# Kernel optimization log

Measured on AMD Instinct MI355X. Metric: run time of the kernel, lower is better.

Reference implementation:

```python
import jax, jax.numpy as jnp
import numpy as np

# e2m1 FP4 value table: sign bit in nibble MSB, values {0,0.5,1,1.5,2,3,4,6}
_E2M1 = jnp.array([0.0, 0.5, 1.0, 1.5, 2.0, 3.0, 4.0, 6.0,
                   -0.0, -0.5, -1.0, -1.5, -2.0, -3.0, -4.0, -6.0], dtype=jnp.float32)


def _dequant_fp4(packed, scales, group_size):
    """packed: [E, out, in//8] uint32; scales: [E, in//group_size, out] -> [E, out, in] f32."""
    shifts = jnp.arange(8, dtype=jnp.uint32) * 4  # nibble shift amounts 0,4,...,28
    nib = (packed[..., None] >> shifts) & jnp.uint32(0xF)  # [E, out, in//8, 8]
    E, O, P, _ = nib.shape
    nib = nib.reshape(E, O, P * 8).astype(jnp.int32)
    w = _E2M1[nib]  # [E, out, in] f32
    gids = jnp.arange(P * 8) // group_size  # group id per input column
    sc = jnp.transpose(scales, (0, 2, 1))[:, :, gids]  # [E, out, in]
    return w * sc


def setup_inputs() -> dict:
    E, H, I, T, K, G = 8, 2048, 1408, 2048, 2, 128
    key = jax.random.key(0)
    ks = jax.random.split(key, 9)
    x = jax.random.normal(ks[0], (T, H), dtype=jnp.float32)
    gate_packed = jax.random.bits(ks[1], (E, I, H // 8), dtype=jnp.uint32)
    up_packed = jax.random.bits(ks[2], (E, I, H // 8), dtype=jnp.uint32)
    down_packed = jax.random.bits(ks[3], (E, H, I // 8), dtype=jnp.uint32)
    gate_scales = jax.random.uniform(ks[4], (E, H // G, I), jnp.float32, 0.5, 1.5)
    up_scales = jax.random.uniform(ks[5], (E, H // G, I), jnp.float32, 0.5, 1.5)
    down_scales = jax.random.uniform(ks[6], (E, I // G, H), jnp.float32, 0.5, 1.5)
    topk_idx = jax.random.randint(ks[7], (T, K), 0, E, dtype=jnp.int32)
    w = jax.random.uniform(ks[8], (T, K), jnp.float32)
    topk_w = w / jnp.sum(w, axis=-1, keepdims=True)
    return {"x": x,
            "gate_packed": gate_packed, "gate_scales": gate_scales,
            "up_packed": up_packed, "up_scales": up_scales,
            "down_packed": down_packed, "down_scales": down_scales,
            "topk_idx": topk_idx, "topk_w": topk_w, "group_size": G}


def reference(x, gate_packed, gate_scales, up_packed, up_scales,
              down_packed, down_scales, topk_idx, topk_w, group_size):
    # Fused dequant (nibble unpack + e2m1 table + per-group scale) for all experts
    gate_w = _dequant_fp4(gate_packed, gate_scales, group_size)  # [E, I, H]
    up_w = _dequant_fp4(up_packed, up_scales, group_size)        # [E, I, H]
    down_w = _dequant_fp4(down_packed, down_scales, group_size)  # [E, H, I]
    # Grouped SwiGLU expert MLP (dense over E=8 experts, gather routed outputs)
    g = jnp.einsum('th,eih->eti', x, gate_w)
    u = jnp.einsum('th,eih->eti', x, up_w)
    h = jax.nn.silu(g) * u                                        # [E, T, I]
    y = jnp.einsum('eti,ehi->eth', h, down_w)                     # [E, T, H]
    T = x.shape[0]
    sel = y[topk_idx, jnp.arange(T)[:, None], :]                  # [T, K, H]
    return jnp.sum(sel * topk_w[..., None], axis=1)               # [T, H]
```

## Files before the change

### kernel.cpp

```cpp
#include <hip/hip_runtime.h>
#include <hip/hip_bf16.h>
#include <stdint.h>

#define E_ 8
#define H_ 2048
#define I_ 1408
#define T_ 2048
#define K_ 2
#define G_ 128

typedef __bf16 bf16;
typedef bf16 bf16x8 __attribute__((ext_vector_type(8)));
typedef float f32x4 __attribute__((ext_vector_type(4)));

__device__ __forceinline__ uint32_t prm(uint32_t hi, uint32_t lo, uint32_t sel) {
    return __builtin_amdgcn_perm(hi, lo, sel);
}

struct DequantTab { uint32_t thi0, thi1, tlo0, tlo1; };

__device__ __forceinline__ DequantTab build_tab(float s) {
    union { bf16 h[8]; uint32_t u[4]; } tb;
    tb.h[0] = (bf16)(0.0f);
    tb.h[1] = (bf16)(0.5f * s);
    tb.h[2] = (bf16)(1.0f * s);
    tb.h[3] = (bf16)(1.5f * s);
    tb.h[4] = (bf16)(2.0f * s);
    tb.h[5] = (bf16)(3.0f * s);
    tb.h[6] = (bf16)(4.0f * s);
    tb.h[7] = (bf16)(6.0f * s);
    DequantTab t;
    t.thi0 = prm(tb.u[1], tb.u[0], 0x07050301u);
    t.tlo0 = prm(tb.u[1], tb.u[0], 0x06040200u);
    t.thi1 = prm(tb.u[3], tb.u[2], 0x07050301u);
    t.tlo1 = prm(tb.u[3], tb.u[2], 0x06040200u);
    return t;
}

__device__ __forceinline__ uint4 dequant8t(uint32_t p, const DequantTab& t) {
    const uint32_t pr = p >> 4;
    const uint32_t pe = p  & 0x07070707u;
    const uint32_t po = pr & 0x07070707u;
    const uint32_t He = prm(t.thi1, t.thi0, pe) | ((p  & 0x08080808u) << 4);
    const uint32_t Le = prm(t.tlo1, t.tlo0, pe);
    const uint32_t Ho = prm(t.thi1, t.thi0, po) | ((pr & 0x08080808u) << 4);
    const uint32_t Lo = prm(t.tlo1, t.tlo0, po);
    const uint32_t E01 = prm(He, Le, 0x05010400u);
    const uint32_t E23 = prm(He, Le, 0x07030602u);
    const uint32_t O01 = prm(Ho, Lo, 0x05010400u);
    const uint32_t O23 = prm(Ho, Lo, 0x07030602u);
    return make_uint4(prm(O01, E01, 0x05040100u),
                      prm(O01, E01, 0x07060302u),
                      prm(O23, E23, 0x05040100u),
                      prm(O23, E23, 0x07060302u));
}

__device__ __forceinline__ void gld16(void* lds, const void* g) {
    __builtin_amdgcn_global_load_lds(
        (__attribute__((address_space(1))) void*)g,
        (__attribute__((address_space(3))) void*)lds, 16, 0, 0);
}

__global__ void route_count(const int* __restrict__ topk_idx, int* __restrict__ counts) {
    int p = blockIdx.x * blockDim.x + threadIdx.x;
    if (p < T_ * K_) atomicAdd(&counts[topk_idx[p]], 1);
}

__global__ void route_scan(const int* __restrict__ counts, int* __restrict__ offsets,
                           int* __restrict__ tmap) {
    if (threadIdx.x == 0) {
        int acc = 0, ti = 0;
        for (int e = 0; e < E_; e++) {
            offsets[e] = acc;
            int nt = (counts[e] + 63) >> 6;
            for (int j = 0; j < nt; j++) tmap[ti++] = (e << 16) | j;
            acc += counts[e];
        }
        offsets[E_] = acc;
        for (; ti < 128; ti++) tmap[ti] = -1;
    }
}

__global__ void route_fill(const int* __restrict__ topk_idx, const float* __restrict__ topk_w,
                           int* __restrict__ cursors, const int* __restrict__ offsets,
                           int* __restrict__ tok, float* __restrict__ wgt,
                           int* __restrict__ inv) {
    int p = blockIdx.x * blockDim.x + threadIdx.x;
    if (p < T_ * K_) {
        int e = topk_idx[p];
        int slot = atomicAdd(&cursors[e], 1);
        int idx = offsets[e] + slot;
        tok[idx] = p / K_;
        wgt[idx] = topk_w[p];
        inv[p] = idx;
    }
}

__global__ __launch_bounds__(256)
void xcast_kernel(const float* __restrict__ x, uint4* __restrict__ xb) {
    const int i = blockIdx.x * 256 + threadIdx.x;
    const float4 a = ((const float4*)x)[i * 2];
    const float4 b = ((const float4*)x)[i * 2 + 1];
    union { uint4 u; bf16 h[8]; } r;
    r.h[0] = (bf16)a.x; r.h[1] = (bf16)a.y; r.h[2] = (bf16)a.z; r.h[3] = (bf16)a.w;
    r.h[4] = (bf16)b.x; r.h[5] = (bf16)b.y; r.h[6] = (bf16)b.z; r.h[7] = (bf16)b.w;
    xb[i] = r.u;
}

__global__ __launch_bounds__(256, 4)
void gemm1t_kernel(const bf16* __restrict__ xb,
                   const uint32_t* __restrict__ gate_packed,
                   const float* __restrict__ gate_scales,
                   const uint32_t* __restrict__ up_packed,
                   const float* __restrict__ up_scales,
                   const int* __restrict__ offsets,
                   const int* __restrict__ tmap,
                   const int* __restrict__ tok, bf16* __restrict__ h_buf)
{
    const int tm = tmap[blockIdx.y];
    if (tm < 0) return;
    const int e = tm >> 16, ty = tm & 0xffff;
    const int row0 = offsets[e];
    const int cnt = offsets[e + 1] - row0;
    const int itile = blockIdx.x;

    __shared__ __align__(16) bf16 xs[64][32];
    __shared__ __align__(16) bf16 wgs[64][32];
    __shared__ __align__(16) bf16 wus[64][32];
    __shared__ int toks[64];

    const int tid = threadIdx.x;
    if (tid < 64) {
        int r = ty * 64 + tid;
        toks[tid] = tok[row0 + ((r < cnt) ? r : (cnt - 1))];
    }
    __syncthreads();

    const int srow = tid >> 2;
    const int scol = (tid & 3) * 8;
    const int wcol = tid & 3;
    const bf16* xg = xb + (size_t)toks[srow] * H_ + scol;
    bf16* lx = &xs[srow][scol];

    const int irow = itile * 64 + srow;
    const uint32_t* gp_row = gate_packed + (size_t)e * I_ * (H_ / 8) + (size_t)irow * (H_ / 8) + wcol;
    const uint32_t* up_row = up_packed + (size_t)e * I_ * (H_ / 8) + (size_t)irow * (H_ / 8) + wcol;
    const float* gs_row = gate_scales + (size_t)e * (H_ / G_) * I_ + irow;
    const float* us_row = up_scales + (size_t)e * (H_ / G_) * I_ + irow;
    uint4* lwg = (uint4*)&wgs[srow][wcol * 8];
    uint4* lwu = (uint4*)&wus[srow][wcol * 8];

    const int wave = tid >> 6, lane = tid & 63;
    const int wy = wave >> 1, wx = wave & 1;
    const int lrow = lane & 15, kq = lane >> 4;

    f32x4 accg[2][2] = {};
    f32x4 accu[2][2] = {};

    for (int kg = 0; kg < H_ / G_; kg++) {
        const DequantTab tg = build_tab(gs_row[kg * I_]);
        const DequantTab tu = build_tab(us_row[kg * I_]);
#pragma unroll
        for (int kk = 0; kk < 4; kk++) {
            const int k0 = kg * 128 + kk * 32;
            gld16(lx, xg + k0);
            const uint32_t pg = gp_row[kg * 16 + kk * 4];
            const uint32_t pu = up_row[kg * 16 + kk * 4];
            *lwg = dequant8t(pg, tg);
            *lwu = dequant8t(pu, tu);
            __syncthreads();

            bf16x8 a[2], bg[2], bu[2];
#pragma unroll
            for (int mi = 0; mi < 2; mi++)
                a[mi] = *(const bf16x8*)&xs[wy * 32 + mi * 16 + lrow][kq * 8];
#pragma unroll
            for (int ni = 0; ni < 2; ni++) {
                bg[ni] = *(const bf16x8*)&wgs[wx * 32 + ni * 16 + lrow][kq * 8];
                bu[ni] = *(const bf16x8*)&wus[wx * 32 + ni * 16 + lrow][kq * 8];
            }
#pragma unroll
            for (int mi = 0; mi < 2; mi++)
#pragma unroll
                for (int ni = 0; ni < 2; ni++) {
                    accg[mi][ni] = __builtin_amdgcn_mfma_f32_16x16x32_bf16(a[mi], bg[ni], accg[mi][ni], 0, 0, 0);
                    accu[mi][ni] = __builtin_amdgcn_mfma_f32_16x16x32_bf16(a[mi], bu[ni], accu[mi][ni], 0, 0, 0);
                }
            __syncthreads();
        }
    }

#pragma unroll
    for (int mi = 0; mi < 2; mi++)
#pragma unroll
        for (int ni = 0; ni < 2; ni++) {
            const int icol = itile * 64 + wx * 32 + ni * 16 + lrow;
#pragma unroll
            for (int r = 0; r < 4; r++) {
                const int grow = ty * 64 + wy * 32 + mi * 16 + kq * 4 + r;
                if (grow < cnt) {
                    const float gv = accg[mi][ni][r];
                    const float hv = gv / (1.f + __expf(-gv)) * accu[mi][ni][r];
                    h_buf[(size_t)(row0 + grow) * I_ + icol] = (bf16)hv;
                }
            }
        }
}

__global__ __launch_bounds__(256, 4)
void gemm2t_kernel(const bf16* __restrict__ h_buf,
                   const uint32_t* __restrict__ down_packed,
                   const float* __restrict__ down_scales,
                   const int* __restrict__ offsets,
                   const int* __restrict__ tmap,
                   const float* __restrict__ wgt, float* __restrict__ yp)
{
    const int tm = tmap[blockIdx.y];
    if (tm < 0) return;
    const int e = tm >> 16, ty = tm & 0xffff;
    const int row0 = offsets[e];
    const int cnt = offsets[e + 1] - row0;
    const int htile = blockIdx.x;

    __shared__ __align__(16) bf16 hs[64][32];
    __shared__ __align__(16) bf16 wds[128][32];
    __shared__ float wgts[64];

    const int tid = threadIdx.x;
    if (tid < 64) {
        int r = ty * 64 + tid;
        wgts[tid] = (r < cnt) ? wgt[row0 + r] : 0.f;
    }
    __syncthreads();

    const int srow = tid >> 2;
    const int scol = (tid & 3) * 8;
    const int m0 = ty * 64 + srow;
    const int hr0 = row0 + ((m0 < cnt) ? m0 : (cnt - 1));
    const bf16* hg = h_buf + (size_t)hr0 * I_ + scol;
    bf16* lh = &hs[srow][scol];

    const int srow2 = tid >> 1;
    const int wcol2 = (tid & 1) * 2;
    const int hrow = htile * 128 + srow2;
    const uint32_t* dp_row = down_packed + (size_t)e * H_ * (I_ / 8) + (size_t)hrow * (I_ / 8) + wcol2;
    const float* ds_row = down_scales + (size_t)e * (I_ / G_) * H_ + hrow;
    uint4* lwd0 = (uint4*)&wds[srow2][wcol2 * 8];
    uint4* lwd1 = (uint4*)&wds[srow2][wcol2 * 8 + 8];

    const int wave = tid >> 6, lane = tid & 63;
    const int wy = wave >> 1, wx = wave & 1;
    const int lrow = lane & 15, kq = lane >> 4;

    f32x4 acc[2][4] = {};

    for (int kg = 0; kg < I_ / G_; kg++) {
        const DequantTab td = build_tab(ds_row[kg * H_]);
#pragma unroll
        for (int kk = 0; kk < 4; kk++) {
            const int k0 = kg * 128 + kk * 32;
            gld16(lh, hg + k0);
            const uint32_t pd0 = dp_row[kg * 16 + kk * 4];
            const uint32_t pd1 = dp_row[kg * 16 + kk * 4 + 1];
            *lwd0 = dequant8t(pd0, td);
            *lwd1 = dequant8t(pd1, td);
            __syncthreads();

            bf16x8 a[2], b[4];
#pragma unroll
            for (int mi = 0; mi < 2; mi++)
                a[mi] = *(const bf16x8*)&hs[wy * 32 + mi * 16 + lrow][kq * 8];
#pragma unroll
            for (int ni = 0; ni < 4; ni++)
                b[ni] = *(const bf16x8*)&wds[wx * 64 + ni * 16 + lrow][kq * 8];
#pragma unroll
            for (int mi = 0; mi < 2; mi++)
#pragma unroll
                for (int ni = 0; ni < 4; ni++)
                    acc[mi][ni] = __builtin_amdgcn_mfma_f32_16x16x32_bf16(a[mi], b[ni], acc[mi][ni], 0, 0, 0);
            __syncthreads();
        }
    }

#pragma unroll
    for (int mi = 0; mi < 2; mi++)
#pragma unroll
        for (int r = 0; r < 4; r++) {
            const int lr = wy * 32 + mi * 16 + kq * 4 + r;
            const int grow = ty * 64 + lr;
            if (grow < cnt) {
                const float w = wgts[lr];
#pragma unroll
                for (int ni = 0; ni < 4; ni++) {
                    const int col = htile * 128 + wx * 64 + ni * 16 + lrow;
                    yp[(size_t)(row0 + grow) * H_ + col] = acc[mi][ni][r] * w;
                }
            }
        }
}

__global__ __launch_bounds__(256)
void combine_kernel(const float* __restrict__ yp, const int* __restrict__ inv,
                    float* __restrict__ out) {
    const int idx = blockIdx.x * 256 + threadIdx.x;
    const int t = idx >> 9;
    const int c = idx & 511;
    const float4 a = ((const float4*)yp)[(size_t)inv[t * 2] * (H_ / 4) + c];
    const float4 b = ((const float4*)yp)[(size_t)inv[t * 2 + 1] * (H_ / 4) + c];
    float4 o;
    o.x = a.x + b.x; o.y = a.y + b.y; o.z = a.z + b.z; o.w = a.w + b.w;
    ((float4*)out)[idx] = o;
}

extern "C" void kernel_launch(void* const* d_in, const int* in_sizes, int n_in,
                              void* d_out, int out_size, void* d_ws, size_t ws_size,
                              hipStream_t stream) {
    const float* x = (const float*)d_in[0];
    const uint32_t* gate_packed = (const uint32_t*)d_in[1];
    const float* gate_scales = (const float*)d_in[2];
    const uint32_t* up_packed = (const uint32_t*)d_in[3];
    const float* up_scales = (const float*)d_in[4];
    const uint32_t* down_packed = (const uint32_t*)d_in[5];
    const float* down_scales = (const float*)d_in[6];
    const int* topk_idx = (const int*)d_in[7];
    const float* topk_w = (const float*)d_in[8];
    float* out = (float*)d_out;

    char* ws = (char*)d_ws;
    int* counts  = (int*)ws;
    int* cursors = (int*)(ws + 32);
    int* offsets = (int*)(ws + 64);
    int* tmap    = (int*)(ws + 128);
    int* tok     = (int*)(ws + 640);
    float* wgt   = (float*)(ws + 17024);
    int* inv     = (int*)(ws + 33408);
    bf16* h_buf  = (bf16*)(ws + 49792);
    bf16* xb     = (bf16*)(ws + 49792 + 11534336ull);
    float* yp    = (float*)(ws + 49792 + 11534336ull + 8388608ull);

    hipMemsetAsync(d_ws, 0, 1024, stream);

    route_count<<<(T_ * K_ + 255) / 256, 256, 0, stream>>>(topk_idx, counts);
    route_scan<<<1, 64, 0, stream>>>(counts, offsets, tmap);
    route_fill<<<(T_ * K_ + 255) / 256, 256, 0, stream>>>(topk_idx, topk_w, cursors, offsets,
                                                          tok, wgt, inv);
    xcast_kernel<<<T_ * H_ / 8 / 256, 256, 0, stream>>>(x, (uint4*)xb);

    dim3 g1(I_ / 64, 72);
    gemm1t_kernel<<<g1, 256, 0, stream>>>(xb, gate_packed, gate_scales, up_packed, up_scales,
                                          offsets, tmap, tok, h_buf);
    dim3 g2(H_ / 128, 72);
    gemm2t_kernel<<<g2, 256, 0, stream>>>(h_buf, down_packed, down_scales,
                                          offsets, tmap, wgt, yp);
    combine_kernel<<<T_ * H_ / 4 / 256, 256, 0, stream>>>(yp, inv, out);
}
```

Before: 306.3 us.

## Double K-step per sync, swizzle LDS layout, vectorize weight loads, swap grid axes

```diff
diff --git a/kernel.cpp b/kernel.cpp
--- a/kernel.cpp
+++ b/kernel.cpp
@@ -117,38 +117,39 @@
                    const int* __restrict__ tmap,
                    const int* __restrict__ tok, bf16* __restrict__ h_buf)
 {
-    const int tm = tmap[blockIdx.y];
+    const int tm = tmap[blockIdx.x];
     if (tm < 0) return;
     const int e = tm >> 16, ty = tm & 0xffff;
     const int row0 = offsets[e];
     const int cnt = offsets[e + 1] - row0;
-    const int itile = blockIdx.x;
-
-    __shared__ __align__(16) bf16 xs[64][32];
-    __shared__ __align__(16) bf16 wgs[64][32];
-    __shared__ __align__(16) bf16 wus[64][32];
-    __shared__ int toks[64];
+    const int itile = blockIdx.y;
+
+    __shared__ __align__(16) bf16 xs[64][64];
+    __shared__ __align__(16) bf16 wgs[64][64];
+    __shared__ __align__(16) bf16 wus[64][64];
 
     const int tid = threadIdx.x;
-    if (tid < 64) {
-        int r = ty * 64 + tid;
-        toks[tid] = tok[row0 + ((r < cnt) ? r : (cnt - 1))];
-    }
-    __syncthreads();
-
-    const int srow = tid >> 2;
-    const int scol = (tid & 3) * 8;
-    const int wcol = tid & 3;
-    const bf16* xg = xb + (size_t)toks[srow] * H_ + scol;
-    bf16* lx = &xs[srow][scol];
-
-    const int irow = itile * 64 + srow;
-    const uint32_t* gp_row = gate_packed + (size_t)e * I_ * (H_ / 8) + (size_t)irow * (H_ / 8) + wcol;
-    const uint32_t* up_row = up_packed + (size_t)e * I_ * (H_ / 8) + (size_t)irow * (H_ / 8) + wcol;
-    const float* gs_row = gate_scales + (size_t)e * (H_ / G_) * I_ + irow;
-    const float* us_row = up_scales + (size_t)e * (H_ / G_) * I_ + irow;
-    uint4* lwg = (uint4*)&wgs[srow][wcol * 8];
-    uint4* lwu = (uint4*)&wus[srow][wcol * 8];
+
+    const int xr0 = tid >> 3;
+    const int xr1 = xr0 + 32;
+    const int xc  = tid & 7;
+    int g0 = ty * 64 + xr0;  g0 = (g0 < cnt) ? g0 : (cnt - 1);
+    int g1 = ty * 64 + xr1;  g1 = (g1 < cnt) ? g1 : (cnt - 1);
+    const bf16* xsrc0 = xb + (size_t)tok[row0 + g0] * H_ + ((xc ^ (xr0 & 7)) * 8);
+    const bf16* xsrc1 = xb + (size_t)tok[row0 + g1] * H_ + ((xc ^ (xr1 & 7)) * 8);
+    bf16* xdst0 = &xs[xr0][xc * 8];
+    bf16* xdst1 = &xs[xr1][xc * 8];
+
+    const int mat  = tid >> 7;
+    const int id   = tid & 127;
+    const int wrow = id >> 1;
+    const int quad = id & 1;
+    const int irow = itile * 64 + wrow;
+    const uint32_t* wp_row = (mat ? up_packed : gate_packed)
+        + (size_t)e * I_ * (H_ / 8) + (size_t)irow * (H_ / 8) + quad * 4;
+    const float* ws_row = (mat ? up_scales : gate_scales)
+        + (size_t)e * (H_ / G_) * I_ + irow;
+    bf16 (* const wdst)[64] = mat ? wus : wgs;
 
     const int wave = tid >> 6, lane = tid & 63;
     const int wy = wave >> 1, wx = wave & 1;
@@ -158,34 +159,49 @@
     f32x4 accu[2][2] = {};
 
     for (int kg = 0; kg < H_ / G_; kg++) {
-        const DequantTab tg = build_tab(gs_row[kg * I_]);
-        const DequantTab tu = build_tab(us_row[kg * I_]);
-#pragma unroll
-        for (int kk = 0; kk < 4; kk++) {
-            const int k0 = kg * 128 + kk * 32;
-            gld16(lx, xg + k0);
-            const uint32_t pg = gp_row[kg * 16 + kk * 4];
-            const uint32_t pu = up_row[kg * 16 + kk * 4];
-            *lwg = dequant8t(pg, tg);
-            *lwu = dequant8t(pu, tu);
+        const DequantTab tw = build_tab(ws_row[kg * I_]);
+#pragma unroll
+        for (int kh2 = 0; kh2 < 2; kh2++) {
+            const int k0 = kg * 128 + kh2 * 64;
+            gld16(xdst0, xsrc0 + k0);
+            gld16(xdst1, xsrc1 + k0);
+            const uint4 pw = *(const uint4*)(wp_row + (k0 >> 3));
+            {
+                uint4 d0 = dequant8t(pw.x, tw);
+                uint4 d1 = dequant8t(pw.y, tw);
+                uint4 d2 = dequant8t(pw.z, tw);
+                uint4 d3 = dequant8t(pw.w, tw);
+                const int cb = quad * 4, rs = wrow & 7;
+                *(uint4*)&wdst[wrow][((cb + 0) ^ rs) * 8] = d0;
+                *(uint4*)&wdst[wrow][((cb + 1) ^ rs) * 8] = d1;
+                *(uint4*)&wdst[wrow][((cb + 2) ^ rs) * 8] = d2;
+                *(uint4*)&wdst[wrow][((cb + 3) ^ rs) * 8] = d3;
+            }
             __syncthreads();
 
-            bf16x8 a[2], bg[2], bu[2];
-#pragma unroll
-            for (int mi = 0; mi < 2; mi++)
-                a[mi] = *(const bf16x8*)&xs[wy * 32 + mi * 16 + lrow][kq * 8];
-#pragma unroll
-            for (int ni = 0; ni < 2; ni++) {
-                bg[ni] = *(const bf16x8*)&wgs[wx * 32 + ni * 16 + lrow][kq * 8];
-                bu[ni] = *(const bf16x8*)&wus[wx * 32 + ni * 16 + lrow][kq * 8];
-            }
-#pragma unroll
-            for (int mi = 0; mi < 2; mi++)
+#pragma unroll
+            for (int kh = 0; kh < 2; kh++) {
+                bf16x8 a[2], bg[2], bu[2];
+#pragma unroll
+                for (int mi = 0; mi < 2; mi++) {
+                    const int ra = wy * 32 + mi * 16 + lrow;
+                    a[mi] = *(const bf16x8*)&xs[ra][((kh * 4 + kq) ^ (ra & 7)) * 8];
+                }
 #pragma unroll
                 for (int ni = 0; ni < 2; ni++) {
-                    accg[mi][ni] = __builtin_amdgcn_mfma_f32_16x16x32_bf16(a[mi], bg[ni], accg[mi][ni], 0, 0, 0);
-                    accu[mi][ni] = __builtin_amdgcn_mfma_f32_16x16x32_bf16(a[mi], bu[ni], accu[mi][ni], 0, 0, 0);
-                }
+                    const int rb = wx * 32 + ni * 16 + lrow;
+                    const int cb = ((kh * 4 + kq) ^ (rb & 7)) * 8;
+                    bg[ni] = *(const bf16x8*)&wgs[rb][cb];
+                    bu[ni] = *(const bf16x8*)&wus[rb][cb];
+                }
+#pragma unroll
+                for (int mi = 0; mi < 2; mi++)
+#pragma unroll
+                    for (int ni = 0; ni < 2; ni++) {
+                        accg[mi][ni] = __builtin_amdgcn_mfma_f32_16x16x32_bf16(a[mi], bg[ni], accg[mi][ni], 0, 0, 0);
+                        accu[mi][ni] = __builtin_amdgcn_mfma_f32_16x16x32_bf16(a[mi], bu[ni], accu[mi][ni], 0, 0, 0);
+                    }
+            }
             __syncthreads();
         }
     }
@@ -215,38 +231,33 @@
                    const int* __restrict__ tmap,
                    const float* __restrict__ wgt, float* __restrict__ yp)
 {
-    const int tm = tmap[blockIdx.y];
+    const int tm = tmap[blockIdx.x];
     if (tm < 0) return;
     const int e = tm >> 16, ty = tm & 0xffff;
     const int row0 = offsets[e];
     const int cnt = offsets[e + 1] - row0;
-    const int htile = blockIdx.x;
-
-    __shared__ __align__(16) bf16 hs[64][32];
-    __shared__ __align__(16) bf16 wds[128][32];
-    __shared__ float wgts[64];
+    const int htile = blockIdx.y;
+
+    __shared__ __align__(16) bf16 hs[64][64];
+    __shared__ __align__(16) bf16 wds[128][64];
 
     const int tid = threadIdx.x;
-    if (tid < 64) {
-        int r = ty * 64 + tid;
-        wgts[tid] = (r < cnt) ? wgt[row0 + r] : 0.f;
-    }
-    __syncthreads();
-
-    const int srow = tid >> 2;
-    const int scol = (tid & 3) * 8;
-    const int m0 = ty * 64 + srow;
-    const int hr0 = row0 + ((m0 < cnt) ? m0 : (cnt - 1));
-    const bf16* hg = h_buf + (size_t)hr0 * I_ + scol;
-    bf16* lh = &hs[srow][scol];
-
-    const int srow2 = tid >> 1;
-    const int wcol2 = (tid & 1) * 2;
-    const int hrow = htile * 128 + srow2;
-    const uint32_t* dp_row = down_packed + (size_t)e * H_ * (I_ / 8) + (size_t)hrow * (I_ / 8) + wcol2;
+
+    const int xr0 = tid >> 3;
+    const int xr1 = xr0 + 32;
+    const int xc  = tid & 7;
+    int g0 = ty * 64 + xr0;  g0 = (g0 < cnt) ? g0 : (cnt - 1);
+    int g1 = ty * 64 + xr1;  g1 = (g1 < cnt) ? g1 : (cnt - 1);
+    const bf16* hsrc0 = h_buf + (size_t)(row0 + g0) * I_ + ((xc ^ (xr0 & 7)) * 8);
+    const bf16* hsrc1 = h_buf + (size_t)(row0 + g1) * I_ + ((xc ^ (xr1 & 7)) * 8);
+    bf16* hdst0 = &hs[xr0][xc * 8];
+    bf16* hdst1 = &hs[xr1][xc * 8];
+
+    const int wrow = tid >> 1;
+    const int quad = tid & 1;
+    const int hrow = htile * 128 + wrow;
+    const uint32_t* dp_row = down_packed + (size_t)e * H_ * (I_ / 8) + (size_t)hrow * (I_ / 8) + quad * 4;
     const float* ds_row = down_scales + (size_t)e * (I_ / G_) * H_ + hrow;
-    uint4* lwd0 = (uint4*)&wds[srow2][wcol2 * 8];
-    uint4* lwd1 = (uint4*)&wds[srow2][wcol2 * 8 + 8];
 
     const int wave = tid >> 6, lane = tid & 63;
     const int wy = wave >> 1, wx = wave & 1;
@@ -257,27 +268,43 @@
     for (int kg = 0; kg < I_ / G_; kg++) {
         const DequantTab td = build_tab(ds_row[kg * H_]);
 #pragma unroll
-        for (int kk = 0; kk < 4; kk++) {
-            const int k0 = kg * 128 + kk * 32;
-            gld16(lh, hg + k0);
-            const uint32_t pd0 = dp_row[kg * 16 + kk * 4];
-            const uint32_t pd1 = dp_row[kg * 16 + kk * 4 + 1];
-            *lwd0 = dequant8t(pd0, td);
-            *lwd1 = dequant8t(pd1, td);
+        for (int kh2 = 0; kh2 < 2; kh2++) {
+            const int k0 = kg * 128 + kh2 * 64;
+            gld16(hdst0, hsrc0 + k0);
+            gld16(hdst1, hsrc1 + k0);
+            const uint4 pw = *(const uint4*)(dp_row + (k0 >> 3));
+            {
+                uint4 d0 = dequant8t(pw.x, td);
+                uint4 d1 = dequant8t(pw.y, td);
+                uint4 d2 = dequant8t(pw.z, td);
+                uint4 d3 = dequant8t(pw.w, td);
+                const int cb = quad * 4, rs = wrow & 7;
+                *(uint4*)&wds[wrow][((cb + 0) ^ rs) * 8] = d0;
+                *(uint4*)&wds[wrow][((cb + 1) ^ rs) * 8] = d1;
+                *(uint4*)&wds[wrow][((cb + 2) ^ rs) * 8] = d2;
+                *(uint4*)&wds[wrow][((cb + 3) ^ rs) * 8] = d3;
+            }
             __syncthreads();
 
-            bf16x8 a[2], b[4];
-#pragma unroll
-            for (int mi = 0; mi < 2; mi++)
-                a[mi] = *(const bf16x8*)&hs[wy * 32 + mi * 16 + lrow][kq * 8];
-#pragma unroll
-            for (int ni = 0; ni < 4; ni++)
-                b[ni] = *(const bf16x8*)&wds[wx * 64 + ni * 16 + lrow][kq * 8];
-#pragma unroll
-            for (int mi = 0; mi < 2; mi++)
-#pragma unroll
-                for (int ni = 0; ni < 4; ni++)
-                    acc[mi][ni] = __builtin_amdgcn_mfma_f32_16x16x32_bf16(a[mi], b[ni], acc[mi][ni], 0, 0, 0);
+#pragma unroll
+            for (int kh = 0; kh < 2; kh++) {
+                bf16x8 a[2], b[4];
+#pragma unroll
+                for (int mi = 0; mi < 2; mi++) {
+                    const int ra = wy * 32 + mi * 16 + lrow;
+                    a[mi] = *(const bf16x8*)&hs[ra][((kh * 4 + kq) ^ (ra & 7)) * 8];
+                }
+#pragma unroll
+                for (int ni = 0; ni < 4; ni++) {
+                    const int rb = wx * 64 + ni * 16 + lrow;
+                    b[ni] = *(const bf16x8*)&wds[rb][((kh * 4 + kq) ^ (rb & 7)) * 8];
+                }
+#pragma unroll
+                for (int mi = 0; mi < 2; mi++)
+#pragma unroll
+                    for (int ni = 0; ni < 4; ni++)
+                        acc[mi][ni] = __builtin_amdgcn_mfma_f32_16x16x32_bf16(a[mi], b[ni], acc[mi][ni], 0, 0, 0);
+            }
             __syncthreads();
         }
     }
@@ -289,7 +316,7 @@
             const int lr = wy * 32 + mi * 16 + kq * 4 + r;
             const int grow = ty * 64 + lr;
             if (grow < cnt) {
-                const float w = wgts[lr];
+                const float w = wgt[row0 + grow];
 #pragma unroll
                 for (int ni = 0; ni < 4; ni++) {
                     const int col = htile * 128 + wx * 64 + ni * 16 + lrow;
@@ -346,10 +373,10 @@
                                                           tok, wgt, inv);
     xcast_kernel<<<T_ * H_ / 8 / 256, 256, 0, stream>>>(x, (uint4*)xb);
 
-    dim3 g1(I_ / 64, 72);
+    dim3 g1(72, I_ / 64);
     gemm1t_kernel<<<g1, 256, 0, stream>>>(xb, gate_packed, gate_scales, up_packed, up_scales,
                                           offsets, tmap, tok, h_buf);
-    dim3 g2(H_ / 128, 72);
+    dim3 g2(72, H_ / 128);
     gemm2t_kernel<<<g2, 256, 0, stream>>>(h_buf, down_packed, down_scales,
                                           offsets, tmap, wgt, yp);
     combine_kernel<<<T_ * H_ / 4 / 256, 256, 0, stream>>>(yp, inv, out);
```

After: 288.2 us. -5.9%, faster.
